# Optimization experiments

Measured on AMD Instinct MI355X. Metric: run time of the kernel, lower is better.

Reference implementation:

```python
import jax, jax.numpy as jnp
import numpy as np

N = 100000
E = 1600000
IN_C = 64
HID = 64
HEADS = 8
HEAD_D = HID // HEADS  # 8
LAYERS = 12
OUT_C = 10
STEPS = 5
NEG_SLOPE = 0.2


def setup_inputs() -> dict:
    key = jax.random.key(0)
    ks = jax.random.split(key, 12)
    x = jax.random.normal(ks[0], (N, IN_C), dtype=jnp.float32)
    edge_index = jax.random.randint(ks[1], (2, E), 0, N, dtype=jnp.int64)
    s = 0.1
    return {
        "x": x,
        "edge_index": edge_index,
        # GAT params: HEADS independent single-head GATConv(in -> HEAD_D)
        "gat_W": jax.random.normal(ks[2], (HEADS, IN_C, HEAD_D), dtype=jnp.float32) * s,
        "gat_a_src": jax.random.normal(ks[3], (HEADS, HEAD_D), dtype=jnp.float32) * s,
        "gat_a_dst": jax.random.normal(ks[4], (HEADS, HEAD_D), dtype=jnp.float32) * s,
        "gat_b": jax.random.normal(ks[5], (HEADS, HEAD_D), dtype=jnp.float32) * s,
        # GCN params: LAYERS x GCNConv(HID -> HID)
        "gcn_W": jax.random.normal(ks[6], (LAYERS, HID, HID), dtype=jnp.float32) * s,
        "gcn_b": jax.random.normal(ks[7], (LAYERS, HID), dtype=jnp.float32) * s,
        # final linear
        "fc_W": jax.random.normal(ks[8], (HID, OUT_C), dtype=jnp.float32) * s,
        "fc_b": jax.random.normal(ks[9], (OUT_C,), dtype=jnp.float32) * s,
    }


def _random_walk(x, row, col):
    # sparse A (COO: row=edge_index[0], col=edge_index[1], vals=1) applied num_steps times
    for _ in range(STEPS):
        x = jax.ops.segment_sum(x[col], row, num_segments=N)
    return x


def _gat_all_heads(x, W, a_src, a_dst, b, src, dst):
    # add self loops
    loop = jnp.arange(N, dtype=src.dtype)
    s2 = jnp.concatenate([src, loop])
    d2 = jnp.concatenate([dst, loop])
    h = jnp.einsum('nf,hfd->nhd', x, W)                      # [N,H,D]
    al_s = jnp.einsum('nhd,hd->nh', h, a_src)                # [N,H]
    al_d = jnp.einsum('nhd,hd->nh', h, a_dst)
    e = jax.nn.leaky_relu(al_s[s2] + al_d[d2], NEG_SLOPE)    # [E+N,H]
    m = jax.ops.segment_max(e, d2, num_segments=N)           # per-target max (self loops -> every node has >=1 edge)
    p = jnp.exp(e - m[d2])
    denom = jax.ops.segment_sum(p, d2, num_segments=N)
    alpha = p / denom[d2]                                    # [E+N,H]
    out = jax.ops.segment_sum(alpha[:, :, None] * h[s2], d2, num_segments=N)  # [N,H,D]
    out = out + b[None, :, :]
    return out.reshape(N, HEADS * HEAD_D)                    # concat heads -> [N,HID]


def _gcn(x, W, b, src, dst):
    loop = jnp.arange(N, dtype=src.dtype)
    s2 = jnp.concatenate([src, loop])
    d2 = jnp.concatenate([dst, loop])
    deg = jax.ops.segment_sum(jnp.ones(s2.shape[0], x.dtype), d2, num_segments=N)
    dis = jnp.where(deg > 0, jax.lax.rsqrt(jnp.maximum(deg, 1.0)), 0.0)
    norm = dis[s2] * dis[d2]                                 # [E+N]
    h = x @ W                                                # [N,HID]
    out = jax.ops.segment_sum(norm[:, None] * h[s2], d2, num_segments=N)
    return out + b


def reference(x, edge_index, gat_W, gat_a_src, gat_a_dst, gat_b, gcn_W, gcn_b, fc_W, fc_b):
    row, col = edge_index[0], edge_index[1]
    # 1) random walk diffusion
    x = _random_walk(x, row, col)
    # 2) multi-head GAT (8 independent heads, concatenated)
    x = _gat_all_heads(x, gat_W, gat_a_src, gat_a_dst, gat_b, row, col)
    # 3) deep residual GCN (faithful to the original indexing quirks)
    initial_residual = x
    for i in range(LAYERS):
        x = _gcn(x, gcn_W[i], gcn_b[i], row, col)
        if i > 0:
            x = x + initial_residual
            initial_residual = x
        x = jax.nn.relu(x)
        if i < LAYERS - 1:
            # note: i-1 == -1 at i==0 -> last layer, as in the torch code
            x = x + _gcn(x, gcn_W[i - 1], gcn_b[i - 1], row, col)
    # 4) final linear
    return x @ fc_W + fc_b
```

## Files before the change

### kernel.cpp

```cpp
#include <hip/hip_runtime.h>


typedef unsigned int u32;

#define BSH 7
#define RNGB 128
#define GEB 256

__device__ __forceinline__ float lrelu(float v) { return v > 0.f ? v : 0.2f * v; }
__device__ __forceinline__ float bf_lo(u32 w) { return __uint_as_float(w << 16); }
__device__ __forceinline__ float bf_hi(u32 w) { return __uint_as_float(w & 0xffff0000u); }
__device__ __forceinline__ u32 pack_bf16(float a, float b) {
  u32 ua = __float_as_uint(a); ua = ua + 0x7fffu + ((ua >> 16) & 1u);
  u32 ub = __float_as_uint(b); ub = ub + 0x7fffu + ((ub >> 16) & 1u);
  return (ua >> 16) | (ub & 0xffff0000u);
}
__device__ __forceinline__ void acc8(float* acc, uint4 q) {
  acc[0] += bf_lo(q.x); acc[1] += bf_hi(q.x);
  acc[2] += bf_lo(q.y); acc[3] += bf_hi(q.y);
  acc[4] += bf_lo(q.z); acc[5] += bf_hi(q.z);
  acc[6] += bf_lo(q.w); acc[7] += bf_hi(q.w);
}
__device__ __forceinline__ void fma8(float* acc, float p, uint4 q) {
  acc[0] = fmaf(p, bf_lo(q.x), acc[0]); acc[1] = fmaf(p, bf_hi(q.x), acc[1]);
// ... 92 lines not shown
    int* __restrict__ idx, float* __restrict__ dis, int N) {
  __shared__ int cnt[RNGB], pfx[RNGB];
  int b = blockIdx.x;
  int node0 = b << BSH;
  int rng = min(RNGB, N - node0);
  int bstart = base[b], bcount = tot[b];
  for (int i = threadIdx.x; i < rng; i += 256) cnt[i] = 0;
  __syncthreads();
  for (int i = threadIdx.x; i < bcount; i += 256) {
    int2 p = pairs[bstart + i];
    int loc = (KEY == 0 ? p.x : p.y) - node0;
    atomicAdd(&cnt[loc], 1);
  }
  __syncthreads();
  if (threadIdx.x == 0) {
    int run = 0;
    for (int i = 0; i < rng; ++i) { pfx[i] = run; run += cnt[i]; }
  }
  __syncthreads();
  for (int i = threadIdx.x; i < rng; i += 256) {
    off[node0 + i] = bstart + pfx[i];
    if (KEY == 1) dis[node0 + i] = rsqrtf((float)(cnt[i] + 1));
  }
  __syncthreads();
  for (int i = threadIdx.x; i < bcount; i += 256) {
    int2 p = pairs[bstart + i];
    int loc = (KEY == 0 ? p.x : p.y) - node0;
    int pos = bstart + atomicAdd(&pfx[loc], 1);
    idx[pos] = (KEY == 0 ? p.y : p.x);
  }
}


__global__ __launch_bounds__(256) void k_gemm64(
    const float* __restrict__ X, const float* __restrict__ W,
    const float* __restrict__ dis, u32* __restrict__ Hb, int n) {
  __shared__ float Xs[64 * 65];
  int row0 = blockIdx.x * 64;
  for (int t = threadIdx.x; t < 1024; t += 256) {
    int r = t >> 4, k4 = t & 15;
    int row = row0 + r;
    float4 v = (row < n) ? ((const float4*)X)[(size_t)row * 16 + k4]
                         : float4{0.f, 0.f, 0.f, 0.f};
    float* dst = &Xs[r * 65 + k4 * 4];
    dst[0] = v.x; dst[1] = v.y; dst[2] = v.z; dst[3] = v.w;
  }
  __syncthreads();
  int lane = threadIdx.x & 63;
  int w = __builtin_amdgcn_readfirstlane(threadIdx.x >> 6);
  int c0 = w * 16;
  int row = row0 + lane;
  float acc[16];
#pragma unroll
  for (int c = 0; c < 16; ++c) acc[c] = 0.f;
#pragma unroll 4
  for (int k = 0; k < 64; ++k) {
    float xk = Xs[lane * 65 + k];
#pragma unroll
    for (int c = 0; c < 16; ++c)
      acc[c] = fmaf(xk, W[k * 64 + c0 + c], acc[c]);
  }
  if (row >= n) return;
  float sc = dis[row];
  uint4* H4 = (uint4*)Hb;
  uint4 o0 = {pack_bf16(acc[0] * sc, acc[1] * sc), pack_bf16(acc[2] * sc, acc[3] * sc),
              pack_bf16(acc[4] * sc, acc[5] * sc), pack_bf16(acc[6] * sc, acc[7] * sc)};
  uint4 o1 = {pack_bf16(acc[8] * sc, acc[9] * sc), pack_bf16(acc[10] * sc, acc[11] * sc),
              pack_bf16(acc[12] * sc, acc[13] * sc), pack_bf16(acc[14] * sc, acc[15] * sc)};
  H4[(size_t)row * 8 + w * 2] = o0;
  H4[(size_t)row * 8 + w * 2 + 1] = o1;
}

__global__ __launch_bounds__(256) void k_gat_gemm(
    const u32* __restrict__ Xb, const float* __restrict__ W,
    const float* __restrict__ asrc, const float* __restrict__ adst,
    u32* __restrict__ Hgb, float* __restrict__ al, int n) {
  __shared__ float Xs[64 * 65];
  int row0 = blockIdx.x * 64;
  for (int t = threadIdx.x; t < 512; t += 256) {
    int r = t >> 3, k8 = t & 7;
    int row = row0 + r;
    uint4 xw = (row < n) ? ((const uint4*)Xb)[(size_t)row * 8 + k8]
                         : uint4{0u, 0u, 0u, 0u};
    float* dst = &Xs[r * 65 + k8 * 8];
    dst[0] = bf_lo(xw.x); dst[1] = bf_hi(xw.x);
    dst[2] = bf_lo(xw.y); dst[3] = bf_hi(xw.y);
    dst[4] = bf_lo(xw.z); dst[5] = bf_hi(xw.z);
    dst[6] = bf_lo(xw.w); dst[7] = bf_hi(xw.w);
  }
  __syncthreads();
  int lane = threadIdx.x & 63;
  int w = __builtin_amdgcn_readfirstlane(threadIdx.x >> 6);
  int c0 = w * 16;
  int row = row0 + lane;
  float acc[16];
#pragma unroll
  for (int c = 0; c < 16; ++c) acc[c] = 0.f;
#pragma unroll 4
  for (int k = 0; k < 64; ++k) {
    float xk = Xs[lane * 65 + k];
#pragma unroll
    for (int c = 0; c < 16; ++c) {
      int gc = c0 + c;
      acc[c] = fmaf(xk, W[(gc >> 3) * 512 + k * 8 + (gc & 7)], acc[c]);
    }
  }
  if (row >= n) return;
  float s1a = 0.f, s2a = 0.f, s1b = 0.f, s2b = 0.f;
#pragma unroll
  for (int cc = 0; cc < 8; ++cc) {
    s1a = fmaf(acc[cc], asrc[c0 + cc], s1a);
    s2a = fmaf(acc[cc], adst[c0 + cc], s2a);
    s1b = fmaf(acc[8 + cc], asrc[c0 + 8 + cc], s1b);
    s2b = fmaf(acc[8 + cc], adst[c0 + 8 + cc], s2b);
  }
  float2* al2 = (float2*)al;
  al2[(size_t)row * 8 + w] = {s1a, s1b};
  al2[(size_t)row * 8 + 4 + w] = {s2a, s2b};
  uint4* H4 = (uint4*)Hgb;
  uint4 o0 = {pack_bf16(acc[0], acc[1]), pack_bf16(acc[2], acc[3]),
              pack_bf16(acc[4], acc[5]), pack_bf16(acc[6], acc[7])};
  uint4 o1 = {pack_bf16(acc[8], acc[9]), pack_bf16(acc[10], acc[11]),
              pack_bf16(acc[12], acc[13]), pack_bf16(acc[14], acc[15])};
  H4[(size_t)row * 8 + w * 2] = o0;
  H4[(size_t)row * 8 + w * 2 + 1] = o1;
}


enum { MODE_RW1 = 0, MODE_RW = 1, MODE_G0 = 2, MODE_GR = 3, MODE_GD = 4 };

template <int MODE>
__global__ __launch_bounds__(256) void k_agg(
    const int* __restrict__ off, const int* __restrict__ idx,
    const float* __restrict__ Hf, const u32* __restrict__ Hb,
    const float* __restrict__ dis, const float* __restrict__ bias,
    float* __restrict__ R, float* __restrict__ Xf, u32* __restrict__ Xb,
    int n) {
  int lane = threadIdx.x & 63;
  int wid = threadIdx.x >> 6;
  int d0 = blockIdx.x * 8 + wid * 2;
  if (d0 >= n) return;
  int d1 = d0 + 1;
  bool has1 = d1 < n;
  int rg = lane >> 3, cg = lane & 7;
  const uint4* H4b = (const uint4*)Hb;
  const float4* H4f = (const float4*)Hf;
  int beg0 = off[d0], end0 = off[d0 + 1];
  int beg1 = has1 ? off[d1] : 0, end1 = has1 ? off[d1 + 1] : 0;
  int cnt0 = end0 - beg0, cnt1 = end1 - beg1;
  int cmax = cnt0 > cnt1 ? cnt0 : cnt1;
  float acc0[8], acc1[8];
#pragma unroll
  for (int i = 0; i < 8; ++i) { acc0[i] = 0.f; acc1[i] = 0.f; }
  for (int base = 0; base < cmax; base += 64) {
    int c0 = cnt0 - base; if (c0 > 64) c0 = 64;
    int c1 = cnt1 - base; if (c1 > 64) c1 = 64;
    int sidx0 = (lane < c0) ? idx[beg0 + base + lane] : -1;
    int sidx1 = (lane < c1) ? idx[beg1 + base + lane] : -1;
    int hi = c0 > c1 ? c0 : c1;
    int nI = (hi + 7) >> 3;
    int j = 0;
    for (; j + 2 <= nI; j += 2) {
      int s00 = __shfl(sidx0, j * 8 + rg, 64);
      int s01 = __shfl(sidx0, j * 8 + 8 + rg, 64);
      int s10 = __shfl(sidx1, j * 8 + rg, 64);
      int s11 = __shfl(sidx1, j * 8 + 8 + rg, 64);
      size_t a00 = (size_t)(s00 >= 0 ? s00 : 0);
      size_t a01 = (size_t)(s01 >= 0 ? s01 : 0);
      size_t a10 = (size_t)(s10 >= 0 ? s10 : 0);
      size_t a11 = (size_t)(s11 >= 0 ? s11 : 0);
      if (MODE == MODE_RW1) {
        float4 x00 = H4f[a00 * 16 + cg * 2], y00 = H4f[a00 * 16 + cg * 2 + 1];
        float4 x01 = H4f[a01 * 16 + cg * 2], y01 = H4f[a01 * 16 + cg * 2 + 1];
        float4 x10 = H4f[a10 * 16 + cg * 2], y10 = H4f[a10 * 16 + cg * 2 + 1];
        float4 x11 = H4f[a11 * 16 + cg * 2], y11 = H4f[a11 * 16 + cg * 2 + 1];
        if (s00 < 0) { x00 = {0,0,0,0}; y00 = {0,0,0,0}; }
        if (s01 < 0) { x01 = {0,0,0,0}; y01 = {0,0,0,0}; }
        if (s10 < 0) { x10 = {0,0,0,0}; y10 = {0,0,0,0}; }
        if (s11 < 0) { x11 = {0,0,0,0}; y11 = {0,0,0,0}; }
        acc0[0] += x00.x; acc0[1] += x00.y; acc0[2] += x00.z; acc0[3] += x00.w;
        acc0[4] += y00.x; acc0[5] += y00.y; acc0[6] += y00.z; acc0[7] += y00.w;
        acc0[0] += x01.x; acc0[1] += x01.y; acc0[2] += x01.z; acc0[3] += x01.w;
        acc0[4] += y01.x; acc0[5] += y01.y; acc0[6] += y01.z; acc0[7] += y01.w;
        acc1[0] += x10.x; acc1[1] += x10.y; acc1[2] += x10.z; acc1[3] += x10.w;
        acc1[4] += y10.x; acc1[5] += y10.y; acc1[6] += y10.z; acc1[7] += y10.w;
        acc1[0] += x11.x; acc1[1] += x11.y; acc1[2] += x11.z; acc1[3] += x11.w;
        acc1[4] += y11.x; acc1[5] += y11.y; acc1[6] += y11.z; acc1[7] += y11.w;
      } else {
        uint4 q00 = H4b[a00 * 8 + cg];
        uint4 q01 = H4b[a01 * 8 + cg];
        uint4 q10 = H4b[a10 * 8 + cg];
        uint4 q11 = H4b[a11 * 8 + cg];
        if (s00 < 0) q00 = {0u,0u,0u,0u};
        if (s01 < 0) q01 = {0u,0u,0u,0u};
        if (s10 < 0) q10 = {0u,0u,0u,0u};
        if (s11 < 0) q11 = {0u,0u,0u,0u};
        acc8(acc0, q00);
        acc8(acc0, q01);
        acc8(acc1, q10);
        acc8(acc1, q11);
      }
    }
    if (j < nI) {
      int s00 = __shfl(sidx0, j * 8 + rg, 64);
      int s10 = __shfl(sidx1, j * 8 + rg, 64);
      size_t a00 = (size_t)(s00 >= 0 ? s00 : 0);
      size_t a10 = (size_t)(s10 >= 0 ? s10 : 0);
      if (MODE == MODE_RW1) {
        float4 x00 = H4f[a00 * 16 + cg * 2], y00 = H4f[a00 * 16 + cg * 2 + 1];
        float4 x10 = H4f[a10 * 16 + cg * 2], y10 = H4f[a10 * 16 + cg * 2 + 1];
        if (s00 < 0) { x00 = {0,0,0,0}; y00 = {0,0,0,0}; }
        if (s10 < 0) { x10 = {0,0,0,0}; y10 = {0,0,0,0}; }
        acc0[0] += x00.x; acc0[1] += x00.y; acc0[2] += x00.z; acc0[3] += x00.w;
        acc0[4] += y00.x; acc0[5] += y00.y; acc0[6] += y00.z; acc0[7] += y00.w;
        acc1[0] += x10.x; acc1[1] += x10.y; acc1[2] += x10.z; acc1[3] += x10.w;
        acc1[4] += y10.x; acc1[5] += y10.y; acc1[6] += y10.z; acc1[7] += y10.w;
      } else {
        uint4 q00 = H4b[a00 * 8 + cg];
        uint4 q10 = H4b[a10 * 8 + cg];
        if (s00 < 0) q00 = {0u,0u,0u,0u};
        if (s10 < 0) q10 = {0u,0u,0u,0u};
        acc8(acc0, q00);
        acc8(acc1, q10);
      }
    }
  }
#pragma unroll
  for (int m = 8; m < 64; m <<= 1)
#pragma unroll
    for (int i = 0; i < 8; ++i) {
      acc0[i] += __shfl_xor(acc0[i], m, 64);
      acc1[i] += __shfl_xor(acc1[i], m, 64);
    }
  if (rg != 0) return;
#pragma unroll
  for (int nd = 0; nd < 2; ++nd) {
    int d = nd == 0 ? d0 : d1;
    if (nd == 1 && !has1) break;
    float* acc = nd == 0 ? acc0 : acc1;
    if (MODE == MODE_RW1 || MODE == MODE_RW) {
      uint4 o = {pack_bf16(acc[0], acc[1]), pack_bf16(acc[2], acc[3]),
                 pack_bf16(acc[4], acc[5]), pack_bf16(acc[6], acc[7])};
      ((uint4*)Xb)[(size_t)d * 8 + cg] = o;
      continue;
    }
    float ddv = dis[d];
    uint4 hw = H4b[(size_t)d * 8 + cg];
    float hs[8] = {bf_lo(hw.x), bf_hi(hw.x), bf_lo(hw.y), bf_hi(hw.y),
                   bf_lo(hw.z), bf_hi(hw.z), bf_lo(hw.w), bf_hi(hw.w)};
    float4 b0 = ((const float4*)bias)[cg * 2];
    float4 b1 = ((const float4*)bias)[cg * 2 + 1];
    float bv[8] = {b0.x, b0.y, b0.z, b0.w, b1.x, b1.y, b1.z, b1.w};
    float v[8];
#pragma unroll
    for (int i = 0; i < 8; ++i) v[i] = ddv * (acc[i] + hs[i]) + bv[i];
    float4* X4 = (float4*)Xf;
    size_t o0 = (size_t)d * 16 + cg * 2;
    if (MODE == MODE_GR) {
      float4* R4 = (float4*)R;
      float4 r0 = R4[o0], r1 = R4[o0 + 1];
      v[0] += r0.x; v[1] += r0.y; v[2] += r0.z; v[3] += r0.w;
      v[4] += r1.x; v[5] += r1.y; v[6] += r1.z; v[7] += r1.w;
      R4[o0] = {v[0], v[1], v[2], v[3]};
      R4[o0 + 1] = {v[4], v[5], v[6], v[7]};
      X4[o0] = {fmaxf(v[0], 0.f), fmaxf(v[1], 0.f), fmaxf(v[2], 0.f), fmaxf(v[3], 0.f)};
      X4[o0 + 1] = {fmaxf(v[4], 0.f), fmaxf(v[5], 0.f), fmaxf(v[6], 0.f), fmaxf(v[7], 0.f)};
    } else if (MODE == MODE_GD) {
      float4 x0 = X4[o0], x1 = X4[o0 + 1];
      X4[o0] = {x0.x + v[0], x0.y + v[1], x0.z + v[2], x0.w + v[3]};
      X4[o0 + 1] = {x1.x + v[4], x1.y + v[5], x1.z + v[6], x1.w + v[7]};
    } else {
      X4[o0] = {fmaxf(v[0], 0.f), fmaxf(v[1], 0.f), fmaxf(v[2], 0.f), fmaxf(v[3], 0.f)};
      X4[o0 + 1] = {fmaxf(v[4], 0.f), fmaxf(v[5], 0.f), fmaxf(v[6], 0.f), fmaxf(v[7], 0.f)};
    }
  }
}

__global__ __launch_bounds__(256) void k_gat_agg(
    const int* __restrict__ off, const int* __restrict__ idx,
    const u32* __restrict__ Hgb, const float* __restrict__ al,
    const float* __restrict__ bias, float* __restrict__ X,
    float* __restrict__ R, int n) {
  int lane = threadIdx.x & 63;
  int wid = threadIdx.x >> 6;
  int d0 = blockIdx.x * 8 + wid * 2;
  if (d0 >= n) return;
  int d1 = d0 + 1;
  bool has1 = d1 < n;
  int rg = lane >> 3, cg = lane & 7;
  const uint4* H4b = (const uint4*)Hgb;
  float ald0 = al[(size_t)d0 * 16 + 8 + cg];
  float es0 = lrelu(al[(size_t)d0 * 16 + cg] + ald0);
  float ald1 = has1 ? al[(size_t)d1 * 16 + 8 + cg] : 0.f;
  float es1 = has1 ? lrelu(al[(size_t)d1 * 16 + cg] + ald1) : 0.f;
  int beg0 = off[d0], end0 = off[d0 + 1];
  int beg1 = has1 ? off[d1] : 0, end1 = has1 ? off[d1 + 1] : 0;
  int cnt0 = end0 - beg0, cnt1 = end1 - beg1;
  int cmax = cnt0 > cnt1 ? cnt0 : cnt1;
  float m0 = es0, m1 = es1;
  for (int base = 0; base < cmax; base += 64) {
    int c0 = cnt0 - base; if (c0 > 64) c0 = 64;
    int c1 = cnt1 - base; if (c1 > 64) c1 = 64;
    int sidx0 = (lane < c0) ? idx[beg0 + base + lane] : -1;
    int sidx1 = (lane < c1) ? idx[beg1 + base + lane] : -1;
    int hi = c0 > c1 ? c0 : c1;
    int nI = (hi + 7) >> 3;
    int j = 0;
    for (; j + 2 <= nI; j += 2) {
      int s00 = __shfl(sidx0, j * 8 + rg, 64);
      int s01 = __shfl(sidx0, j * 8 + 8 + rg, 64);
      int s10 = __shfl(sidx1, j * 8 + rg, 64);
      int s11 = __shfl(sidx1, j * 8 + 8 + rg, 64);
      float a00 = al[(size_t)(s00 >= 0 ? s00 : 0) * 16 + cg];
      float a01 = al[(size_t)(s01 >= 0 ? s01 : 0) * 16 + cg];
      float a10 = al[(size_t)(s10 >= 0 ? s10 : 0) * 16 + cg];
      float a11 = al[(size_t)(s11 >= 0 ? s11 : 0) * 16 + cg];
      if (s00 >= 0) m0 = fmaxf(m0, lrelu(a00 + ald0));
      if (s01 >= 0) m0 = fmaxf(m0, lrelu(a01 + ald0));
      if (s10 >= 0) m1 = fmaxf(m1, lrelu(a10 + ald1));
      if (s11 >= 0) m1 = fmaxf(m1, lrelu(a11 + ald1));
    }
    if (j < nI) {
      int s00 = __shfl(sidx0, j * 8 + rg, 64);
      int s10 = __shfl(sidx1, j * 8 + rg, 64);
      float a00 = al[(size_t)(s00 >= 0 ? s00 : 0) * 16 + cg];
      float a10 = al[(size_t)(s10 >= 0 ? s10 : 0) * 16 + cg];
      if (s00 >= 0) m0 = fmaxf(m0, lrelu(a00 + ald0));
      if (s10 >= 0) m1 = fmaxf(m1, lrelu(a10 + ald1));
    }
  }
#pragma unroll
  for (int mm = 8; mm < 64; mm <<= 1) {
    m0 = fmaxf(m0, __shfl_xor(m0, mm, 64));
    m1 = fmaxf(m1, __shfl_xor(m1, mm, 64));
  }
  float den0 = 0.f, den1 = 0.f;
  float acc0[8], acc1[8];
#pragma unroll
  for (int i = 0; i < 8; ++i) { acc0[i] = 0.f; acc1[i] = 0.f; }
  for (int base = 0; base < cmax; base += 64) {
    int c0 = cnt0 - base; if (c0 > 64) c0 = 64;
    int c1 = cnt1 - base; if (c1 > 64) c1 = 64;
    int sidx0 = (lane < c0) ? idx[beg0 + base + lane] : -1;
    int sidx1 = (lane < c1) ? idx[beg1 + base + lane] : -1;
    int hi = c0 > c1 ? c0 : c1;
    int nI = (hi + 7) >> 3;
    int j = 0;
    for (; j + 2 <= nI; j += 2) {
      int s00 = __shfl(sidx0, j * 8 + rg, 64);
      int s01 = __shfl(sidx0, j * 8 + 8 + rg, 64);
      int s10 = __shfl(sidx1, j * 8 + rg, 64);
      int s11 = __shfl(sidx1, j * 8 + 8 + rg, 64);
      size_t a00 = (size_t)(s00 >= 0 ? s00 : 0);
      size_t a01 = (size_t)(s01 >= 0 ? s01 : 0);
      size_t a10 = (size_t)(s10 >= 0 ? s10 : 0);
      size_t a11 = (size_t)(s11 >= 0 ? s11 : 0);
      float l00 = al[a00 * 16 + cg];
      float l01 = al[a01 * 16 + cg];
      float l10 = al[a10 * 16 + cg];
      float l11 = al[a11 * 16 + cg];
      uint4 q00 = H4b[a00 * 8 + cg];
      uint4 q01 = H4b[a01 * 8 + cg];
      uint4 q10 = H4b[a10 * 8 + cg];
      uint4 q11 = H4b[a11 * 8 + cg];
      float p00 = (s00 >= 0) ? __expf(lrelu(l00 + ald0) - m0) : 0.f;
      float p01 = (s01 >= 0) ? __expf(lrelu(l01 + ald0) - m0) : 0.f;
      float p10 = (s10 >= 0) ? __expf(lrelu(l10 + ald1) - m1) : 0.f;
      float p11 = (s11 >= 0) ? __expf(lrelu(l11 + ald1) - m1) : 0.f;
      den0 += p00; fma8(acc0, p00, q00);
      den0 += p01; fma8(acc0, p01, q01);
      den1 += p10; fma8(acc1, p10, q10);
      den1 += p11; fma8(acc1, p11, q11);
    }
    if (j < nI) {
      int s00 = __shfl(sidx0, j * 8 + rg, 64);
      int s10 = __shfl(sidx1, j * 8 + rg, 64);
      size_t a00 = (size_t)(s00 >= 0 ? s00 : 0);
      size_t a10 = (size_t)(s10 >= 0 ? s10 : 0);
      float l00 = al[a00 * 16 + cg];
      float l10 = al[a10 * 16 + cg];
      uint4 q00 = H4b[a00 * 8 + cg];
      uint4 q10 = H4b[a10 * 8 + cg];
      float p00 = (s00 >= 0) ? __expf(lrelu(l00 + ald0) - m0) : 0.f;
      float p10 = (s10 >= 0) ? __expf(lrelu(l10 + ald1) - m1) : 0.f;
      den0 += p00; fma8(acc0, p00, q00);
      den1 += p10; fma8(acc1, p10, q10);
    }
  }
#pragma unroll
  for (int mm = 8; mm < 64; mm <<= 1) {
#pragma unroll
    for (int i = 0; i < 8; ++i) {
      acc0[i] += __shfl_xor(acc0[i], mm, 64);
      acc1[i] += __shfl_xor(acc1[i], mm, 64);
    }
    den0 += __shfl_xor(den0, mm, 64);
    den1 += __shfl_xor(den1, mm, 64);
  }
  if (rg != 0) return;
#pragma unroll
  for (int nd = 0; nd < 2; ++nd) {
    if (nd == 1 && !has1) break;
    int d = nd == 0 ? d0 : d1;
    float* acc = nd == 0 ? acc0 : acc1;
    float es = nd == 0 ? es0 : es1;
    float m = nd == 0 ? m0 : m1;
    float den = nd == 0 ? den0 : den1;
    float pself = __expf(es - m);
    uint4 hw = H4b[(size_t)d * 8 + cg];
    float hs[8] = {bf_lo(hw.x), bf_hi(hw.x), bf_lo(hw.y), bf_hi(hw.y),
                   bf_lo(hw.z), bf_hi(hw.z), bf_lo(hw.w), bf_hi(hw.w)};
#pragma unroll
    for (int i = 0; i < 8; ++i) acc[i] = fmaf(pself, hs[i], acc[i]);
    den += pself;
    float inv = 1.f / den;
    float4 b0 = ((const float4*)bias)[cg * 2];
    float4 b1 = ((const float4*)bias)[cg * 2 + 1];
    float bv[8] = {b0.x, b0.y, b0.z, b0.w, b1.x, b1.y, b1.z, b1.w};
    float v[8];
#pragma unroll
    for (int i = 0; i < 8; ++i) v[i] = acc[i] * inv + bv[i];
    size_t o0 = (size_t)d * 16 + cg * 2;
    ((float4*)X)[o0] = {v[0], v[1], v[2], v[3]};
    ((float4*)X)[o0 + 1] = {v[4], v[5], v[6], v[7]};
    ((float4*)R)[o0] = {v[0], v[1], v[2], v[3]};
    ((float4*)R)[o0 + 1] = {v[4], v[5], v[6], v[7]};
  }
}


__global__ __launch_bounds__(256) void k_fc(
    const float* __restrict__ X, const float* __restrict__ W,
    const float* __restrict__ b, float* __restrict__ out, int n) {
  __shared__ float Wl[640];
  __shared__ float bl[10];
  for (int i = threadIdx.x; i < 640; i += 256) Wl[i] = W[i];
  if (threadIdx.x < 10) bl[threadIdx.x] = b[threadIdx.x];
  __syncthreads();
  int r = blockIdx.x * blockDim.x + threadIdx.x;
  if (r >= n) return;
  float acc[10];
#pragma unroll
  for (int c = 0; c < 10; ++c) acc[c] = bl[c];
#pragma unroll
  for (int k = 0; k < 64; ++k) {
    float xv = X[(size_t)r * 64 + k];
#pragma unroll
    for (int c = 0; c < 10; ++c) acc[c] = fmaf(xv, Wl[k * 10 + c], acc[c]);
  }
#pragma unroll
  for (int c = 0; c < 10; ++c) out[(size_t)r * 10 + c] = acc[c];
}


extern "C" void kernel_launch(void* const* d_in, const int* in_sizes, int n_in,
                              void* d_out, int out_size, void* d_ws, size_t ws_size,
                              hipStream_t stream) {
  const float* x_in  = (const float*)d_in[0];
  const int*   ei    = (const int*)d_in[1];
// ... 21 lines not shown
  };
  int* offA    = (int*)alloc((size_t)(N + 1) * 4);
  int* offB    = (int*)alloc((size_t)(N + 1) * 4);
  float* dis   = (float*)alloc((size_t)N * 4);
  int* idxA    = (int*)alloc((size_t)E * 4);
  int* idxB    = (int*)alloc((size_t)E * 4);
  int2* pairsA = (int2*)alloc((size_t)E * 8);
  int2* pairsB = (int2*)alloc((size_t)E * 8);
  int* gHistA  = (int*)alloc((size_t)GEB * NB * 4);
  int* gHistB  = (int*)alloc((size_t)GEB * NB * 4);
  int* totA    = (int*)alloc((size_t)NB * 4);
  int* totB    = (int*)alloc((size_t)NB * 4);
  int* baseA   = (int*)alloc((size_t)NB * 4);
  int* baseB   = (int*)alloc((size_t)NB * 4);
  float* al    = (float*)alloc((size_t)N * 16 * 4);
  u32* B0      = (u32*)alloc((size_t)N * 32 * 4);
  u32* B1      = (u32*)alloc((size_t)N * 32 * 4);
  float* X     = (float*)alloc((size_t)N * 64 * 4);
  float* R     = (float*)alloc((size_t)N * 64 * 4);

  int nbN = (N + 255) / 256;
  int nbAgg = (N + 7) / 8;
  int nbG = (N + 63) / 64;

  k_hist<<<GEB, 256, 0, stream>>>(ei, E, NB, chunk, gHistA, gHistB);
  k_colscan<<<NB, GEB, 0, stream>>>(gHistA, totA, NB);
  k_colscan<<<NB, GEB, 0, stream>>>(gHistB, totB, NB);
  k_bscan<<<1, 1024, 0, stream>>>(totA, totB, baseA, baseB, offA, offB, NB, N, E);
  k_scatter<<<GEB, 256, 0, stream>>>(ei, E, NB, chunk, gHistA, gHistB,
                                     baseA, baseB, pairsA, pairsB);
  k_bucket<0><<<NB, 256, 0, stream>>>(pairsA, baseA, totA, offA, idxA, nullptr, N);
  k_bucket<1><<<NB, 256, 0, stream>>>(pairsB, baseB, totB, offB, idxB, dis, N);

  k_agg<MODE_RW1><<<nbAgg, 256, 0, stream>>>(offA, idxA, x_in, nullptr, nullptr, nullptr, nullptr, nullptr, B0, N);
  k_agg<MODE_RW><<<nbAgg, 256, 0, stream>>>(offA, idxA, nullptr, B0, nullptr, nullptr, nullptr, nullptr, B1, N);
  k_agg<MODE_RW><<<nbAgg, 256, 0, stream>>>(offA, idxA, nullptr, B1, nullptr, nullptr, nullptr, nullptr, B0, N);
  k_agg<MODE_RW><<<nbAgg, 256, 0, stream>>>(offA, idxA, nullptr, B0, nullptr, nullptr, nullptr, nullptr, B1, N);
  k_agg<MODE_RW><<<nbAgg, 256, 0, stream>>>(offA, idxA, nullptr, B1, nullptr, nullptr, nullptr, nullptr, B0, N);

  k_gat_gemm<<<nbG, 256, 0, stream>>>(B0, gatW, gatAs, gatAd, B1, al, N);
  k_gat_agg<<<nbAgg, 256, 0, stream>>>(offB, idxB, B1, al, gatB, X, R, N);

  for (int i = 0; i < 12; ++i) {
    k_gemm64<<<nbG, 256, 0, stream>>>(X, gcnW + i * 4096, dis, B0, N);
    if (i == 0)
      k_agg<MODE_G0><<<nbAgg, 256, 0, stream>>>(offB, idxB, nullptr, B0, dis, gcnB + i * 64, nullptr, X, nullptr, N);
    else
      k_agg<MODE_GR><<<nbAgg, 256, 0, stream>>>(offB, idxB, nullptr, B0, dis, gcnB + i * 64, R, X, nullptr, N);
    if (i < 11) {
      int j = (i == 0) ? 11 : i - 1;
      k_gemm64<<<nbG, 256, 0, stream>>>(X, gcnW + j * 4096, dis, B0, N);
      k_agg<MODE_GD><<<nbAgg, 256, 0, stream>>>(offB, idxB, nullptr, B0, dis, gcnB + j * 64, nullptr, X, nullptr, N);
    }
  }

  k_fc<<<nbN, 256, 0, stream>>>(X, fcW, fcB, out, N);
}
```

Measured before the change: 1.776 ms.

## Fuse GCN dense transform into aggregation by aggregating before multiplying by W

Reorders each GCN layer from gemm-then-aggregate to aggregate-then-gemm, using linearity: neighbors' dis-scaled features are gathered in bf16, then multiplied by W inside the same kernel via shared memory. Each conv kernel also emits the next layer's dis-scaled bf16 input, so the separate k_gemm64 launches and their full-matrix write/read round trips are eliminated. This roughly halves the kernel launches in the GCN stack and removes a large amount of memory traffic. It costs a per-wave 64x64 matvec read from global W and adds bf16 rounding at a different point in the computation.

```diff
diff --git a/kernel.cpp b/kernel.cpp
--- a/kernel.cpp
+++ b/kernel.cpp
@@ -148,110 +148,11 @@
 }
 
 
-__global__ __launch_bounds__(256) void k_gemm64(
-    const float* __restrict__ X, const float* __restrict__ W,
-    const float* __restrict__ dis, u32* __restrict__ Hb, int n) {
-  __shared__ float Xs[64 * 65];
-  int row0 = blockIdx.x * 64;
-  for (int t = threadIdx.x; t < 1024; t += 256) {
-    int r = t >> 4, k4 = t & 15;
-    int row = row0 + r;
-    float4 v = (row < n) ? ((const float4*)X)[(size_t)row * 16 + k4]
-                         : float4{0.f, 0.f, 0.f, 0.f};
-    float* dst = &Xs[r * 65 + k4 * 4];
-    dst[0] = v.x; dst[1] = v.y; dst[2] = v.z; dst[3] = v.w;
-  }
-  __syncthreads();
-  int lane = threadIdx.x & 63;
-  int w = __builtin_amdgcn_readfirstlane(threadIdx.x >> 6);
-  int c0 = w * 16;
-  int row = row0 + lane;
-  float acc[16];
-#pragma unroll
-  for (int c = 0; c < 16; ++c) acc[c] = 0.f;
-#pragma unroll 4
-  for (int k = 0; k < 64; ++k) {
-    float xk = Xs[lane * 65 + k];
-#pragma unroll
-    for (int c = 0; c < 16; ++c)
-      acc[c] = fmaf(xk, W[k * 64 + c0 + c], acc[c]);
-  }
-  if (row >= n) return;
-  float sc = dis[row];
-  uint4* H4 = (uint4*)Hb;
-  uint4 o0 = {pack_bf16(acc[0] * sc, acc[1] * sc), pack_bf16(acc[2] * sc, acc[3] * sc),
-              pack_bf16(acc[4] * sc, acc[5] * sc), pack_bf16(acc[6] * sc, acc[7] * sc)};
-  uint4 o1 = {pack_bf16(acc[8] * sc, acc[9] * sc), pack_bf16(acc[10] * sc, acc[11] * sc),
-              pack_bf16(acc[12] * sc, acc[13] * sc), pack_bf16(acc[14] * sc, acc[15] * sc)};
-  H4[(size_t)row * 8 + w * 2] = o0;
-  H4[(size_t)row * 8 + w * 2 + 1] = o1;
-}
-
-__global__ __launch_bounds__(256) void k_gat_gemm(
-    const u32* __restrict__ Xb, const float* __restrict__ W,
-    const float* __restrict__ asrc, const float* __restrict__ adst,
-    u32* __restrict__ Hgb, float* __restrict__ al, int n) {
-  __shared__ float Xs[64 * 65];
-  int row0 = blockIdx.x * 64;
-  for (int t = threadIdx.x; t < 512; t += 256) {
-    int r = t >> 3, k8 = t & 7;
-    int row = row0 + r;
-    uint4 xw = (row < n) ? ((const uint4*)Xb)[(size_t)row * 8 + k8]
-                         : uint4{0u, 0u, 0u, 0u};
-    float* dst = &Xs[r * 65 + k8 * 8];
-    dst[0] = bf_lo(xw.x); dst[1] = bf_hi(xw.x);
-    dst[2] = bf_lo(xw.y); dst[3] = bf_hi(xw.y);
-    dst[4] = bf_lo(xw.z); dst[5] = bf_hi(xw.z);
-    dst[6] = bf_lo(xw.w); dst[7] = bf_hi(xw.w);
-  }
-  __syncthreads();
-  int lane = threadIdx.x & 63;
-  int w = __builtin_amdgcn_readfirstlane(threadIdx.x >> 6);
-  int c0 = w * 16;
-  int row = row0 + lane;
-  float acc[16];
-#pragma unroll
-  for (int c = 0; c < 16; ++c) acc[c] = 0.f;
-#pragma unroll 4
-  for (int k = 0; k < 64; ++k) {
-    float xk = Xs[lane * 65 + k];
-#pragma unroll
-    for (int c = 0; c < 16; ++c) {
-      int gc = c0 + c;
-      acc[c] = fmaf(xk, W[(gc >> 3) * 512 + k * 8 + (gc & 7)], acc[c]);
-    }
-  }
-  if (row >= n) return;
-  float s1a = 0.f, s2a = 0.f, s1b = 0.f, s2b = 0.f;
-#pragma unroll
-  for (int cc = 0; cc < 8; ++cc) {
-    s1a = fmaf(acc[cc], asrc[c0 + cc], s1a);
-    s2a = fmaf(acc[cc], adst[c0 + cc], s2a);
-    s1b = fmaf(acc[8 + cc], asrc[c0 + 8 + cc], s1b);
-    s2b = fmaf(acc[8 + cc], adst[c0 + 8 + cc], s2b);
-  }
-  float2* al2 = (float2*)al;
-  al2[(size_t)row * 8 + w] = {s1a, s1b};
-  al2[(size_t)row * 8 + 4 + w] = {s2a, s2b};
-  uint4* H4 = (uint4*)Hgb;
-  uint4 o0 = {pack_bf16(acc[0], acc[1]), pack_bf16(acc[2], acc[3]),
-              pack_bf16(acc[4], acc[5]), pack_bf16(acc[6], acc[7])};
-  uint4 o1 = {pack_bf16(acc[8], acc[9]), pack_bf16(acc[10], acc[11]),
-              pack_bf16(acc[12], acc[13]), pack_bf16(acc[14], acc[15])};
-  H4[(size_t)row * 8 + w * 2] = o0;
-  H4[(size_t)row * 8 + w * 2 + 1] = o1;
-}
-
-
-enum { MODE_RW1 = 0, MODE_RW = 1, MODE_G0 = 2, MODE_GR = 3, MODE_GD = 4 };
-
-template <int MODE>
-__global__ __launch_bounds__(256) void k_agg(
+template <int FIRST>
+__global__ __launch_bounds__(256) void k_rw(
     const int* __restrict__ off, const int* __restrict__ idx,
     const float* __restrict__ Hf, const u32* __restrict__ Hb,
-    const float* __restrict__ dis, const float* __restrict__ bias,
-    float* __restrict__ R, float* __restrict__ Xf, u32* __restrict__ Xb,
-    int n) {
+    u32* __restrict__ Xb, int n) {
   int lane = threadIdx.x & 63;
   int wid = threadIdx.x >> 6;
   int d0 = blockIdx.x * 8 + wid * 2;
@@ -285,7 +186,7 @@
       size_t a01 = (size_t)(s01 >= 0 ? s01 : 0);
       size_t a10 = (size_t)(s10 >= 0 ? s10 : 0);
       size_t a11 = (size_t)(s11 >= 0 ? s11 : 0);
-      if (MODE == MODE_RW1) {
+      if (FIRST) {
         float4 x00 = H4f[a00 * 16 + cg * 2], y00 = H4f[a00 * 16 + cg * 2 + 1];
         float4 x01 = H4f[a01 * 16 + cg * 2], y01 = H4f[a01 * 16 + cg * 2 + 1];
         float4 x10 = H4f[a10 * 16 + cg * 2], y10 = H4f[a10 * 16 + cg * 2 + 1];
@@ -322,7 +223,7 @@
       int s10 = __shfl(sidx1, j * 8 + rg, 64);
       size_t a00 = (size_t)(s00 >= 0 ? s00 : 0);
       size_t a10 = (size_t)(s10 >= 0 ? s10 : 0);
-      if (MODE == MODE_RW1) {
+      if (FIRST) {
         float4 x00 = H4f[a00 * 16 + cg * 2], y00 = H4f[a00 * 16 + cg * 2 + 1];
         float4 x10 = H4f[a10 * 16 + cg * 2], y10 = H4f[a10 * 16 + cg * 2 + 1];
         if (s00 < 0) { x00 = {0,0,0,0}; y00 = {0,0,0,0}; }
@@ -349,54 +250,77 @@
       acc1[i] += __shfl_xor(acc1[i], m, 64);
     }
   if (rg != 0) return;
-#pragma unroll
-  for (int nd = 0; nd < 2; ++nd) {
-    int d = nd == 0 ? d0 : d1;
-    if (nd == 1 && !has1) break;
-    float* acc = nd == 0 ? acc0 : acc1;
-    if (MODE == MODE_RW1 || MODE == MODE_RW) {
-      uint4 o = {pack_bf16(acc[0], acc[1]), pack_bf16(acc[2], acc[3]),
-                 pack_bf16(acc[4], acc[5]), pack_bf16(acc[6], acc[7])};
-      ((uint4*)Xb)[(size_t)d * 8 + cg] = o;
-      continue;
-    }
-    float ddv = dis[d];
-    uint4 hw = H4b[(size_t)d * 8 + cg];
-    float hs[8] = {bf_lo(hw.x), bf_hi(hw.x), bf_lo(hw.y), bf_hi(hw.y),
-                   bf_lo(hw.z), bf_hi(hw.z), bf_lo(hw.w), bf_hi(hw.w)};
-    float4 b0 = ((const float4*)bias)[cg * 2];
-    float4 b1 = ((const float4*)bias)[cg * 2 + 1];
-    float bv[8] = {b0.x, b0.y, b0.z, b0.w, b1.x, b1.y, b1.z, b1.w};
-    float v[8];
-#pragma unroll
-    for (int i = 0; i < 8; ++i) v[i] = ddv * (acc[i] + hs[i]) + bv[i];
-    float4* X4 = (float4*)Xf;
-    size_t o0 = (size_t)d * 16 + cg * 2;
-    if (MODE == MODE_GR) {
-      float4* R4 = (float4*)R;
-      float4 r0 = R4[o0], r1 = R4[o0 + 1];
-      v[0] += r0.x; v[1] += r0.y; v[2] += r0.z; v[3] += r0.w;
-      v[4] += r1.x; v[5] += r1.y; v[6] += r1.z; v[7] += r1.w;
-      R4[o0] = {v[0], v[1], v[2], v[3]};
-      R4[o0 + 1] = {v[4], v[5], v[6], v[7]};
-      X4[o0] = {fmaxf(v[0], 0.f), fmaxf(v[1], 0.f), fmaxf(v[2], 0.f), fmaxf(v[3], 0.f)};
-      X4[o0 + 1] = {fmaxf(v[4], 0.f), fmaxf(v[5], 0.f), fmaxf(v[6], 0.f), fmaxf(v[7], 0.f)};
-    } else if (MODE == MODE_GD) {
-      float4 x0 = X4[o0], x1 = X4[o0 + 1];
-      X4[o0] = {x0.x + v[0], x0.y + v[1], x0.z + v[2], x0.w + v[3]};
-      X4[o0 + 1] = {x1.x + v[4], x1.y + v[5], x1.z + v[6], x1.w + v[7]};
-    } else {
-      X4[o0] = {fmaxf(v[0], 0.f), fmaxf(v[1], 0.f), fmaxf(v[2], 0.f), fmaxf(v[3], 0.f)};
-      X4[o0 + 1] = {fmaxf(v[4], 0.f), fmaxf(v[5], 0.f), fmaxf(v[6], 0.f), fmaxf(v[7], 0.f)};
-    }
-  }
+  uint4 o0 = {pack_bf16(acc0[0], acc0[1]), pack_bf16(acc0[2], acc0[3]),
+              pack_bf16(acc0[4], acc0[5]), pack_bf16(acc0[6], acc0[7])};
+  ((uint4*)Xb)[(size_t)d0 * 8 + cg] = o0;
+  if (has1) {
+    uint4 o1 = {pack_bf16(acc1[0], acc1[1]), pack_bf16(acc1[2], acc1[3]),
+                pack_bf16(acc1[4], acc1[5]), pack_bf16(acc1[6], acc1[7])};
+    ((uint4*)Xb)[(size_t)d1 * 8 + cg] = o1;
+  }
+}
+
+
+__global__ __launch_bounds__(256) void k_gat_gemm(
+    const u32* __restrict__ Xb, const float* __restrict__ W,
+    const float* __restrict__ asrc, const float* __restrict__ adst,
+    u32* __restrict__ Hgb, float* __restrict__ al, int n) {
+  __shared__ float Xs[64 * 65];
+  int row0 = blockIdx.x * 64;
+  for (int t = threadIdx.x; t < 512; t += 256) {
+    int r = t >> 3, k8 = t & 7;
+    int row = row0 + r;
+    uint4 xw = (row < n) ? ((const uint4*)Xb)[(size_t)row * 8 + k8]
+                         : uint4{0u, 0u, 0u, 0u};
+    float* dst = &Xs[r * 65 + k8 * 8];
+    dst[0] = bf_lo(xw.x); dst[1] = bf_hi(xw.x);
+    dst[2] = bf_lo(xw.y); dst[3] = bf_hi(xw.y);
+    dst[4] = bf_lo(xw.z); dst[5] = bf_hi(xw.z);
+    dst[6] = bf_lo(xw.w); dst[7] = bf_hi(xw.w);
+  }
+  __syncthreads();
+  int lane = threadIdx.x & 63;
+  int w = __builtin_amdgcn_readfirstlane(threadIdx.x >> 6);
+  int c0 = w * 16;
+  int row = row0 + lane;
+  float acc[16];
+#pragma unroll
+  for (int c = 0; c < 16; ++c) acc[c] = 0.f;
+#pragma unroll 4
+  for (int k = 0; k < 64; ++k) {
+    float xk = Xs[lane * 65 + k];
+#pragma unroll
+    for (int c = 0; c < 16; ++c) {
+      int gc = c0 + c;
+      acc[c] = fmaf(xk, W[(gc >> 3) * 512 + k * 8 + (gc & 7)], acc[c]);
+    }
+  }
+  if (row >= n) return;
+  float s1a = 0.f, s2a = 0.f, s1b = 0.f, s2b = 0.f;
+#pragma unroll
+  for (int cc = 0; cc < 8; ++cc) {
+    s1a = fmaf(acc[cc], asrc[c0 + cc], s1a);
+    s2a = fmaf(acc[cc], adst[c0 + cc], s2a);
+    s1b = fmaf(acc[8 + cc], asrc[c0 + 8 + cc], s1b);
+    s2b = fmaf(acc[8 + cc], adst[c0 + 8 + cc], s2b);
+  }
+  float2* al2 = (float2*)al;
+  al2[(size_t)row * 8 + w] = {s1a, s1b};
+  al2[(size_t)row * 8 + 4 + w] = {s2a, s2b};
+  uint4* H4 = (uint4*)Hgb;
+  uint4 o0 = {pack_bf16(acc[0], acc[1]), pack_bf16(acc[2], acc[3]),
+              pack_bf16(acc[4], acc[5]), pack_bf16(acc[6], acc[7])};
+  uint4 o1 = {pack_bf16(acc[8], acc[9]), pack_bf16(acc[10], acc[11]),
+              pack_bf16(acc[12], acc[13]), pack_bf16(acc[14], acc[15])};
+  H4[(size_t)row * 8 + w * 2] = o0;
+  H4[(size_t)row * 8 + w * 2 + 1] = o1;
 }
 
 __global__ __launch_bounds__(256) void k_gat_agg(
     const int* __restrict__ off, const int* __restrict__ idx,
     const u32* __restrict__ Hgb, const float* __restrict__ al,
-    const float* __restrict__ bias, float* __restrict__ X,
-    float* __restrict__ R, int n) {
+    const float* __restrict__ bias, const float* __restrict__ dis,
+    u32* __restrict__ Tout, float* __restrict__ R, int n) {
   int lane = threadIdx.x & 63;
   int wid = threadIdx.x >> 6;
   int d0 = blockIdx.x * 8 + wid * 2;
@@ -537,10 +461,154 @@
 #pragma unroll
     for (int i = 0; i < 8; ++i) v[i] = acc[i] * inv + bv[i];
     size_t o0 = (size_t)d * 16 + cg * 2;
-    ((float4*)X)[o0] = {v[0], v[1], v[2], v[3]};
-    ((float4*)X)[o0 + 1] = {v[4], v[5], v[6], v[7]};
     ((float4*)R)[o0] = {v[0], v[1], v[2], v[3]};
     ((float4*)R)[o0 + 1] = {v[4], v[5], v[6], v[7]};
+    float dd = dis[d];
+    uint4 tw = {pack_bf16(dd * v[0], dd * v[1]), pack_bf16(dd * v[2], dd * v[3]),
+                pack_bf16(dd * v[4], dd * v[5]), pack_bf16(dd * v[6], dd * v[7])};
+    ((uint4*)Tout)[(size_t)d * 8 + cg] = tw;
+  }
+}
+
+
+enum { CG0 = 0, CGR = 1, CGRL = 2, CGD = 3 };
+
+template <int MODE>
+__global__ __launch_bounds__(256) void k_conv(
+    const int* __restrict__ off, const int* __restrict__ idx,
+    const u32* __restrict__ Tin, u32* __restrict__ Tout,
+    const float* __restrict__ dis, const float* __restrict__ W,
+    const float* __restrict__ bias, float* __restrict__ R,
+    float* __restrict__ X, int n) {
+  __shared__ float zs[4][128];
+  int lane = threadIdx.x & 63;
+  int wid = threadIdx.x >> 6;
+  int d0 = blockIdx.x * 8 + wid * 2;
+  if (d0 >= n) return;
+  int d1 = d0 + 1;
+  bool has1 = d1 < n;
+  int rg = lane >> 3, cg = lane & 7;
+  const uint4* T4 = (const uint4*)Tin;
+  int beg0 = off[d0], end0 = off[d0 + 1];
+  int beg1 = has1 ? off[d1] : 0, end1 = has1 ? off[d1 + 1] : 0;
+  int cnt0 = end0 - beg0, cnt1 = end1 - beg1;
+  int cmax = cnt0 > cnt1 ? cnt0 : cnt1;
+  float acc0[8], acc1[8];
+#pragma unroll
+  for (int i = 0; i < 8; ++i) { acc0[i] = 0.f; acc1[i] = 0.f; }
+  for (int base = 0; base < cmax; base += 64) {
+    int c0 = cnt0 - base; if (c0 > 64) c0 = 64;
+    int c1 = cnt1 - base; if (c1 > 64) c1 = 64;
+    int sidx0 = (lane < c0) ? idx[beg0 + base + lane] : -1;
+    int sidx1 = (lane < c1) ? idx[beg1 + base + lane] : -1;
+    int hi = c0 > c1 ? c0 : c1;
+    int nI = (hi + 7) >> 3;
+    int j = 0;
+    for (; j + 2 <= nI; j += 2) {
+      int s00 = __shfl(sidx0, j * 8 + rg, 64);
+      int s01 = __shfl(sidx0, j * 8 + 8 + rg, 64);
+      int s10 = __shfl(sidx1, j * 8 + rg, 64);
+      int s11 = __shfl(sidx1, j * 8 + 8 + rg, 64);
+      size_t a00 = (size_t)(s00 >= 0 ? s00 : 0);
+      size_t a01 = (size_t)(s01 >= 0 ? s01 : 0);
+      size_t a10 = (size_t)(s10 >= 0 ? s10 : 0);
+      size_t a11 = (size_t)(s11 >= 0 ? s11 : 0);
+      uint4 q00 = T4[a00 * 8 + cg];
+      uint4 q01 = T4[a01 * 8 + cg];
+      uint4 q10 = T4[a10 * 8 + cg];
+      uint4 q11 = T4[a11 * 8 + cg];
+      if (s00 < 0) q00 = {0u,0u,0u,0u};
+      if (s01 < 0) q01 = {0u,0u,0u,0u};
+      if (s10 < 0) q10 = {0u,0u,0u,0u};
+      if (s11 < 0) q11 = {0u,0u,0u,0u};
+      acc8(acc0, q00);
+      acc8(acc0, q01);
+      acc8(acc1, q10);
+      acc8(acc1, q11);
+    }
+    if (j < nI) {
+      int s00 = __shfl(sidx0, j * 8 + rg, 64);
+      int s10 = __shfl(sidx1, j * 8 + rg, 64);
+      size_t a00 = (size_t)(s00 >= 0 ? s00 : 0);
+      size_t a10 = (size_t)(s10 >= 0 ? s10 : 0);
+      uint4 q00 = T4[a00 * 8 + cg];
+      uint4 q10 = T4[a10 * 8 + cg];
+      if (s00 < 0) q00 = {0u,0u,0u,0u};
+      if (s10 < 0) q10 = {0u,0u,0u,0u};
+      acc8(acc0, q00);
+      acc8(acc1, q10);
+    }
+  }
+#pragma unroll
+  for (int m = 8; m < 64; m <<= 1)
+#pragma unroll
+    for (int i = 0; i < 8; ++i) {
+      acc0[i] += __shfl_xor(acc0[i], m, 64);
+      acc1[i] += __shfl_xor(acc1[i], m, 64);
+    }
+  float dd0 = dis[d0];
+  uint4 ts0 = T4[(size_t)d0 * 8 + cg];
+  float z0[8] = {dd0 * (acc0[0] + bf_lo(ts0.x)), dd0 * (acc0[1] + bf_hi(ts0.x)),
+                 dd0 * (acc0[2] + bf_lo(ts0.y)), dd0 * (acc0[3] + bf_hi(ts0.y)),
+                 dd0 * (acc0[4] + bf_lo(ts0.z)), dd0 * (acc0[5] + bf_hi(ts0.z)),
+                 dd0 * (acc0[6] + bf_lo(ts0.w)), dd0 * (acc0[7] + bf_hi(ts0.w))};
+  float dd1 = has1 ? dis[d1] : 0.f;
+  uint4 ts1 = T4[(size_t)(has1 ? d1 : d0) * 8 + cg];
+  float z1[8] = {dd1 * (acc1[0] + bf_lo(ts1.x)), dd1 * (acc1[1] + bf_hi(ts1.x)),
+                 dd1 * (acc1[2] + bf_lo(ts1.y)), dd1 * (acc1[3] + bf_hi(ts1.y)),
+                 dd1 * (acc1[4] + bf_lo(ts1.z)), dd1 * (acc1[5] + bf_hi(ts1.z)),
+                 dd1 * (acc1[6] + bf_lo(ts1.w)), dd1 * (acc1[7] + bf_hi(ts1.w))};
+  if (rg == 0) {
+    float4* zp = (float4*)&zs[wid][cg * 8];
+    zp[0] = {z0[0], z0[1], z0[2], z0[3]};
+    zp[1] = {z0[4], z0[5], z0[6], z0[7]};
+    float4* zq = (float4*)&zs[wid][64 + cg * 8];
+    zq[0] = {z1[0], z1[1], z1[2], z1[3]};
+    zq[1] = {z1[4], z1[5], z1[6], z1[7]};
+  }
+  asm volatile("s_waitcnt lgkmcnt(0)" ::: "memory");
+  float outc0 = bias[lane];
+  float outc1 = outc0;
+  const float4* za = (const float4*)&zs[wid][0];
+  const float4* zb = (const float4*)&zs[wid][64];
+#pragma unroll 4
+  for (int k4 = 0; k4 < 16; ++k4) {
+    float4 a = za[k4];
+    float4 b = zb[k4];
+    int k = k4 * 4;
+    float w0 = W[(k + 0) * 64 + lane];
+    float w1 = W[(k + 1) * 64 + lane];
+    float w2 = W[(k + 2) * 64 + lane];
+    float w3 = W[(k + 3) * 64 + lane];
+    outc0 = fmaf(a.x, w0, outc0); outc1 = fmaf(b.x, w0, outc1);
+    outc0 = fmaf(a.y, w1, outc0); outc1 = fmaf(b.y, w1, outc1);
+    outc0 = fmaf(a.z, w2, outc0); outc1 = fmaf(b.z, w2, outc1);
+    outc0 = fmaf(a.w, w3, outc0); outc1 = fmaf(b.w, w3, outc1);
+  }
+#pragma unroll
+  for (int nd = 0; nd < 2; ++nd) {
+    if (nd == 1 && !has1) break;
+    int d = nd == 0 ? d0 : d1;
+    float outv = nd == 0 ? outc0 : outc1;
+    size_t o = (size_t)d * 64 + lane;
+    float res;
+    if (MODE == CGD) {
+      res = X[o] + outv;
+    } else if (MODE == CG0) {
+      res = fmaxf(outv, 0.f);
+      X[o] = res;
+    } else {
+      float val = outv + R[o];
+      R[o] = val;
+      res = fmaxf(val, 0.f);
+      X[o] = res;
+    }
+    if (MODE != CGRL) {
+      float t = dis[d] * res;
+      float tp = __shfl_xor(t, 1, 64);
+      if (!(lane & 1))
+        Tout[(size_t)d * 32 + (lane >> 1)] = pack_bf16(t, tp);
+    }
   }
 }
 
@@ -628,25 +696,33 @@
   k_bucket<0><<<NB, 256, 0, stream>>>(pairsA, baseA, totA, offA, idxA, nullptr, N);
   k_bucket<1><<<NB, 256, 0, stream>>>(pairsB, baseB, totB, offB, idxB, dis, N);
 
-  k_agg<MODE_RW1><<<nbAgg, 256, 0, stream>>>(offA, idxA, x_in, nullptr, nullptr, nullptr, nullptr, nullptr, B0, N);
-  k_agg<MODE_RW><<<nbAgg, 256, 0, stream>>>(offA, idxA, nullptr, B0, nullptr, nullptr, nullptr, nullptr, B1, N);
-  k_agg<MODE_RW><<<nbAgg, 256, 0, stream>>>(offA, idxA, nullptr, B1, nullptr, nullptr, nullptr, nullptr, B0, N);
-  k_agg<MODE_RW><<<nbAgg, 256, 0, stream>>>(offA, idxA, nullptr, B0, nullptr, nullptr, nullptr, nullptr, B1, N);
-  k_agg<MODE_RW><<<nbAgg, 256, 0, stream>>>(offA, idxA, nullptr, B1, nullptr, nullptr, nullptr, nullptr, B0, N);
+  k_rw<1><<<nbAgg, 256, 0, stream>>>(offA, idxA, x_in, nullptr, B0, N);
+  k_rw<0><<<nbAgg, 256, 0, stream>>>(offA, idxA, nullptr, B0, B1, N);
+  k_rw<0><<<nbAgg, 256, 0, stream>>>(offA, idxA, nullptr, B1, B0, N);
+  k_rw<0><<<nbAgg, 256, 0, stream>>>(offA, idxA, nullptr, B0, B1, N);
+  k_rw<0><<<nbAgg, 256, 0, stream>>>(offA, idxA, nullptr, B1, B0, N);
 
   k_gat_gemm<<<nbG, 256, 0, stream>>>(B0, gatW, gatAs, gatAd, B1, al, N);
-  k_gat_agg<<<nbAgg, 256, 0, stream>>>(offB, idxB, B1, al, gatB, X, R, N);
-
+  k_gat_agg<<<nbAgg, 256, 0, stream>>>(offB, idxB, B1, al, gatB, dis, B0, R, N);
+
+  u32* Tc = B0;
+  u32* Ta = B1;
   for (int i = 0; i < 12; ++i) {
-    k_gemm64<<<nbG, 256, 0, stream>>>(X, gcnW + i * 4096, dis, B0, N);
     if (i == 0)
-      k_agg<MODE_G0><<<nbAgg, 256, 0, stream>>>(offB, idxB, nullptr, B0, dis, gcnB + i * 64, nullptr, X, nullptr, N);
+      k_conv<CG0><<<nbAgg, 256, 0, stream>>>(offB, idxB, Tc, Ta, dis,
+                                             gcnW, gcnB, nullptr, X, N);
+    else if (i == 11)
+      k_conv<CGRL><<<nbAgg, 256, 0, stream>>>(offB, idxB, Tc, nullptr, dis,
+                                              gcnW + i * 4096, gcnB + i * 64, R, X, N);
     else
-      k_agg<MODE_GR><<<nbAgg, 256, 0, stream>>>(offB, idxB, nullptr, B0, dis, gcnB + i * 64, R, X, nullptr, N);
+      k_conv<CGR><<<nbAgg, 256, 0, stream>>>(offB, idxB, Tc, Ta, dis,
+                                             gcnW + i * 4096, gcnB + i * 64, R, X, N);
+    { u32* t = Tc; Tc = Ta; Ta = t; }
     if (i < 11) {
       int j = (i == 0) ? 11 : i - 1;
-      k_gemm64<<<nbG, 256, 0, stream>>>(X, gcnW + j * 4096, dis, B0, N);
-      k_agg<MODE_GD><<<nbAgg, 256, 0, stream>>>(offB, idxB, nullptr, B0, dis, gcnB + j * 64, nullptr, X, nullptr, N);
+      k_conv<CGD><<<nbAgg, 256, 0, stream>>>(offB, idxB, Tc, Ta, dis,
+                                             gcnW + j * 4096, gcnB + j * 64, nullptr, X, N);
+      u32* t = Tc; Tc = Ta; Ta = t;
     }
   }
 
```

New measurement: 1.895 ms. 1.07x slower.

## Use online softmax in GAT aggregation to drop separate max pass

Applied to the files above, without the earlier changes.

Replaces the two-pass GAT softmax (a max pass over all neighbors, then an exp/accumulate pass) with a single-pass online softmax that keeps a running max and rescales the accumulator and denominator whenever the max grows. The cross-lane reduction now merges (max, den, acc) triples with rescaling. This removes the second read of edge indices and per-source attention logits, at the cost of divergent rescale branches and extra exp/multiply work in the reduction.

```diff
diff --git a/kernel.cpp b/kernel.cpp
--- a/kernel.cpp
+++ b/kernel.cpp
@@ -413,43 +413,8 @@
   int beg1 = has1 ? off[d1] : 0, end1 = has1 ? off[d1 + 1] : 0;
   int cnt0 = end0 - beg0, cnt1 = end1 - beg1;
   int cmax = cnt0 > cnt1 ? cnt0 : cnt1;
+  const float NEG = -3.0e38f;
   float m0 = es0, m1 = es1;
-  for (int base = 0; base < cmax; base += 64) {
-    int c0 = cnt0 - base; if (c0 > 64) c0 = 64;
-    int c1 = cnt1 - base; if (c1 > 64) c1 = 64;
-    int sidx0 = (lane < c0) ? idx[beg0 + base + lane] : -1;
-    int sidx1 = (lane < c1) ? idx[beg1 + base + lane] : -1;
-    int hi = c0 > c1 ? c0 : c1;
-    int nI = (hi + 7) >> 3;
-    int j = 0;
-    for (; j + 2 <= nI; j += 2) {
-      int s00 = __shfl(sidx0, j * 8 + rg, 64);
-      int s01 = __shfl(sidx0, j * 8 + 8 + rg, 64);
-      int s10 = __shfl(sidx1, j * 8 + rg, 64);
-      int s11 = __shfl(sidx1, j * 8 + 8 + rg, 64);
-      float a00 = al[(size_t)(s00 >= 0 ? s00 : 0) * 16 + cg];
-      float a01 = al[(size_t)(s01 >= 0 ? s01 : 0) * 16 + cg];
-      float a10 = al[(size_t)(s10 >= 0 ? s10 : 0) * 16 + cg];
-      float a11 = al[(size_t)(s11 >= 0 ? s11 : 0) * 16 + cg];
-      if (s00 >= 0) m0 = fmaxf(m0, lrelu(a00 + ald0));
-      if (s01 >= 0) m0 = fmaxf(m0, lrelu(a01 + ald0));
-      if (s10 >= 0) m1 = fmaxf(m1, lrelu(a10 + ald1));
-      if (s11 >= 0) m1 = fmaxf(m1, lrelu(a11 + ald1));
-    }
-    if (j < nI) {
-      int s00 = __shfl(sidx0, j * 8 + rg, 64);
-      int s10 = __shfl(sidx1, j * 8 + rg, 64);
-      float a00 = al[(size_t)(s00 >= 0 ? s00 : 0) * 16 + cg];
-      float a10 = al[(size_t)(s10 >= 0 ? s10 : 0) * 16 + cg];
-      if (s00 >= 0) m0 = fmaxf(m0, lrelu(a00 + ald0));
-      if (s10 >= 0) m1 = fmaxf(m1, lrelu(a10 + ald1));
-    }
-  }
-#pragma unroll
-  for (int mm = 8; mm < 64; mm <<= 1) {
-    m0 = fmaxf(m0, __shfl_xor(m0, mm, 64));
-    m1 = fmaxf(m1, __shfl_xor(m1, mm, 64));
-  }
   float den0 = 0.f, den1 = 0.f;
   float acc0[8], acc1[8];
 #pragma unroll
@@ -479,12 +444,32 @@
       uint4 q01 = H4b[a01 * 8 + cg];
       uint4 q10 = H4b[a10 * 8 + cg];
       uint4 q11 = H4b[a11 * 8 + cg];
-      float p00 = (s00 >= 0) ? __expf(lrelu(l00 + ald0) - m0) : 0.f;
-      float p01 = (s01 >= 0) ? __expf(lrelu(l01 + ald0) - m0) : 0.f;
-      float p10 = (s10 >= 0) ? __expf(lrelu(l10 + ald1) - m1) : 0.f;
-      float p11 = (s11 >= 0) ? __expf(lrelu(l11 + ald1) - m1) : 0.f;
+      float e00 = (s00 >= 0) ? lrelu(l00 + ald0) : NEG;
+      float e01 = (s01 >= 0) ? lrelu(l01 + ald0) : NEG;
+      float e10 = (s10 >= 0) ? lrelu(l10 + ald1) : NEG;
+      float e11 = (s11 >= 0) ? lrelu(l11 + ald1) : NEG;
+      float ml0 = fmaxf(e00, e01);
+      if (ml0 > m0) {
+        float sc = __expf(m0 - ml0);
+        den0 *= sc;
+#pragma unroll
+        for (int i = 0; i < 8; ++i) acc0[i] *= sc;
+        m0 = ml0;
+      }
+      float p00 = (s00 >= 0) ? __expf(e00 - m0) : 0.f;
+      float p01 = (s01 >= 0) ? __expf(e01 - m0) : 0.f;
       den0 += p00; fma8(acc0, p00, q00);
       den0 += p01; fma8(acc0, p01, q01);
+      float ml1 = fmaxf(e10, e11);
+      if (ml1 > m1) {
+        float sc = __expf(m1 - ml1);
+        den1 *= sc;
+#pragma unroll
+        for (int i = 0; i < 8; ++i) acc1[i] *= sc;
+        m1 = ml1;
+      }
+      float p10 = (s10 >= 0) ? __expf(e10 - m1) : 0.f;
+      float p11 = (s11 >= 0) ? __expf(e11 - m1) : 0.f;
       den1 += p10; fma8(acc1, p10, q10);
       den1 += p11; fma8(acc1, p11, q11);
     }
@@ -497,21 +482,52 @@
       float l10 = al[a10 * 16 + cg];
       uint4 q00 = H4b[a00 * 8 + cg];
       uint4 q10 = H4b[a10 * 8 + cg];
-      float p00 = (s00 >= 0) ? __expf(lrelu(l00 + ald0) - m0) : 0.f;
-      float p10 = (s10 >= 0) ? __expf(lrelu(l10 + ald1) - m1) : 0.f;
+      float e00 = (s00 >= 0) ? lrelu(l00 + ald0) : NEG;
+      float e10 = (s10 >= 0) ? lrelu(l10 + ald1) : NEG;
+      if (e00 > m0) {
+        float sc = __expf(m0 - e00);
+        den0 *= sc;
+#pragma unroll
+        for (int i = 0; i < 8; ++i) acc0[i] *= sc;
+        m0 = e00;
+      }
+      float p00 = (s00 >= 0) ? __expf(e00 - m0) : 0.f;
       den0 += p00; fma8(acc0, p00, q00);
+      if (e10 > m1) {
+        float sc = __expf(m1 - e10);
+        den1 *= sc;
+#pragma unroll
+        for (int i = 0; i < 8; ++i) acc1[i] *= sc;
+        m1 = e10;
+      }
+      float p10 = (s10 >= 0) ? __expf(e10 - m1) : 0.f;
       den1 += p10; fma8(acc1, p10, q10);
     }
   }
 #pragma unroll
   for (int mm = 8; mm < 64; mm <<= 1) {
+    float mo0 = __shfl_xor(m0, mm, 64);
+    float do0 = __shfl_xor(den0, mm, 64);
+    float mo1 = __shfl_xor(m1, mm, 64);
+    float do1 = __shfl_xor(den1, mm, 64);
+    float ao0[8], ao1[8];
 #pragma unroll
     for (int i = 0; i < 8; ++i) {
-      acc0[i] += __shfl_xor(acc0[i], mm, 64);
-      acc1[i] += __shfl_xor(acc1[i], mm, 64);
-    }
-    den0 += __shfl_xor(den0, mm, 64);
-    den1 += __shfl_xor(den1, mm, 64);
+      ao0[i] = __shfl_xor(acc0[i], mm, 64);
+      ao1[i] = __shfl_xor(acc1[i], mm, 64);
+    }
+    float mn0 = fmaxf(m0, mo0);
+    float sA0 = __expf(m0 - mn0), sB0 = __expf(mo0 - mn0);
+    den0 = den0 * sA0 + do0 * sB0;
+#pragma unroll
+    for (int i = 0; i < 8; ++i) acc0[i] = acc0[i] * sA0 + ao0[i] * sB0;
+    m0 = mn0;
+    float mn1 = fmaxf(m1, mo1);
+    float sA1 = __expf(m1 - mn1), sB1 = __expf(mo1 - mn1);
+    den1 = den1 * sA1 + do1 * sB1;
+#pragma unroll
+    for (int i = 0; i < 8; ++i) acc1[i] = acc1[i] * sA1 + ao1[i] * sB1;
+    m1 = mn1;
   }
   if (rg != 0) return;
 #pragma unroll
```

After: 1.768 ms. Within noise of the previous version (-0.5%).
